# Optimization experiments

Measured on AMD Instinct MI355X. Metric: run time of the kernel, lower is better.

The kernel has to match this reference:

```python
import jax, jax.numpy as jnp
import numpy as np

EPS = 1e-5

def binary_activation(x):
    # ReActNet piecewise-polynomial STE: forward = sign(x), grad follows poly
    m1 = (x < -1).astype(x.dtype)
    m2 = (x < 0).astype(x.dtype)
    m3 = (x < 1).astype(x.dtype)
    out1 = -1.0 * m1 + (x * x + 2.0 * x) * (1.0 - m1)
    out2 = out1 * m2 + (-x * x + 2.0 * x) * (1.0 - m2)
    out3 = out2 * m3 + 1.0 * (1.0 - m3)
    return jax.lax.stop_gradient(jnp.sign(x) - out3) + out3

def binary_conv(x, w, stride, padding):
    # per-output-channel scaled sign weights with clamp STE
    scale = jnp.mean(jnp.abs(w), axis=(1, 2, 3), keepdims=True)
    clipped = jnp.clip(w, -1.0, 1.0)
    bw = jax.lax.stop_gradient(scale * jnp.sign(w) - clipped) + clipped
    return jax.lax.conv_general_dilated(
        x, bw, window_strides=(stride, stride),
        padding=[(padding, padding), (padding, padding)],
        dimension_numbers=('NCHW', 'OIHW', 'NCHW'))

def batch_norm(x, g, b):
    mu = jnp.mean(x, axis=(0, 2, 3), keepdims=True)
    var = jnp.mean((x - mu) ** 2, axis=(0, 2, 3), keepdims=True)
    xn = (x - mu) * jax.lax.rsqrt(var + EPS)
    return xn * g[None, :, None, None] + b[None, :, None, None]

def prelu(x, a):
    a = a[None, :, None, None]
    return jnp.where(x >= 0, x, a * x)

def setup_inputs() -> dict:
    key = jax.random.key(0)
    ks = jax.random.split(key, 12)
    N, C, H, W = 32, 256, 56, 56
    d = {
        'x': jax.random.normal(ks[0], (N, C, H, W), jnp.float32),
        'b11': jax.random.normal(ks[1], (1, C, 1, 1), jnp.float32) * 0.1,
        'b12': jax.random.normal(ks[2], (1, C, 1, 1), jnp.float32) * 0.1,
        'b13': jax.random.normal(ks[3], (1, C, 1, 1), jnp.float32) * 0.1,
        'b21': jax.random.normal(ks[4], (1, C, 1, 1), jnp.float32) * 0.1,
        'b22': jax.random.normal(ks[5], (1, C, 1, 1), jnp.float32) * 0.1,
        'b23': jax.random.normal(ks[6], (1, C, 1, 1), jnp.float32) * 0.1,
        'w3x3': jax.random.normal(ks[7], (C, C, 3, 3), jnp.float32) * 0.05,
        'wpw': jax.random.normal(ks[8], (C, C, 1, 1), jnp.float32) * 0.05,
        'g1': jnp.ones((C,), jnp.float32),
        'be1': jnp.zeros((C,), jnp.float32),
        'g2': jnp.ones((C,), jnp.float32),
        'be2': jnp.zeros((C,), jnp.float32),
        'p1': jnp.full((C,), 0.25, jnp.float32),
        'p2': jnp.full((C,), 0.25, jnp.float32),
    }
    return d

def reference(x, b11, b12, b13, b21, b22, b23, w3x3, wpw, g1, be1, g2, be2, p1, p2):
    # stride=1, inplanes == planes branch
    out1 = binary_activation(x + b11)
    out1 = binary_conv(out1, w3x3, stride=1, padding=1)
    out1 = batch_norm(out1, g1, be1)
    out1 = x + out1
    out1 = prelu(out1 + b12, p1) + b13
    out2 = binary_activation(out1 + b21)
    out2 = binary_conv(out2, wpw, stride=1, padding=0)
    out2 = batch_norm(out2, g2, be2)
    out2 = out2 + out1
    out2 = prelu(out2 + b22, p2) + b23
    return out2
```

## Files before the change

kernel.cpp:

```cpp
#include <hip/hip_runtime.h>

typedef __attribute__((ext_vector_type(4))) float  f32x4;
typedef __attribute__((ext_vector_type(8))) short  s16x8;
typedef __attribute__((ext_vector_type(4))) short  s16x4;
typedef __attribute__((ext_vector_type(4))) int    i32x4;

#define MFMA16(a, b, c) __builtin_amdgcn_mfma_f32_16x16x32_bf16((a), (b), (c), 0, 0, 0)

__device__ __forceinline__ void gload_lds16(const void* g, void* l) {
  __builtin_amdgcn_global_load_lds((const __attribute__((address_space(1))) void*)g,
                                   (__attribute__((address_space(3))) void*)l, 16, 0, 0);
}

__device__ __forceinline__ unsigned short sgnbits(float v) {
  return v > 0.f ? (unsigned short)0x3F80u : (v < 0.f ? (unsigned short)0xBF80u : (unsigned short)0u);
}

__global__ __launch_bounds__(256) void prep_w(const float* __restrict__ w3,
                                              const float* __restrict__ wpw,
                                              unsigned short* __restrict__ w1s,
                                              unsigned short* __restrict__ w2s,
                                              float* __restrict__ scale1,
                                              float* __restrict__ scale2) {
  const int o = blockIdx.x;
  const int t = threadIdx.x;
  float s = 0.f;
  if (blockIdx.y == 0) {
    for (int u = t; u < 2304; u += 256) {
      int i = u / 9, tap = u % 9;
      float v = w3[(size_t)(o * 256 + i) * 9 + tap];
      s += fabsf(v);
      w1s[(size_t)(tap * 256 + o) * 256 + i] = sgnbits(v);
    }
  } else {
    float v = wpw[o * 256 + t];
    s = fabsf(v);
    w2s[o * 256 + t] = sgnbits(v);
  }
  for (int m = 1; m < 64; m <<= 1) s += __shfl_xor(s, m);
  __shared__ float red[4];
  if ((t & 63) == 0) red[t >> 6] = s;
  __syncthreads();
  if (t == 0) {
    float tot = red[0] + red[1] + red[2] + red[3];
    if (blockIdx.y == 0) scale1[o] = tot / 2304.f;
    else                 scale2[o] = tot / 256.f;
  }
}

__global__ __launch_bounds__(256) void sign_nhwc(const float* __restrict__ x,
                                                 const float* __restrict__ b11,
                                                 unsigned short* __restrict__ out) {
  __shared__ unsigned short l[56 * 256];
  __shared__ float cB[256];
  const int h = blockIdx.x, n = blockIdx.y, t = threadIdx.x;
  cB[t] = b11[t];
  __syncthreads();
  const int wv = t & 15, cg = t >> 4;
  if (wv < 14) {
    const int w0 = wv * 4;
    const int swz = (wv & 7) << 3;
#pragma unroll 4
    for (int it = 0; it < 16; ++it) {
      int c = it * 16 + cg;
      size_t idx = (size_t)(n * 256 + c) * 3136 + h * 56 + w0;
      f32x4 xv = *(const f32x4*)(x + idx);
      float bb = cB[c];
      int cs = c ^ swz;
      l[(w0 + 0) * 256 + cs] = sgnbits(xv[0] + bb);
      l[(w0 + 1) * 256 + cs] = sgnbits(xv[1] + bb);
      l[(w0 + 2) * 256 + cs] = sgnbits(xv[2] + bb);
      l[(w0 + 3) * 256 + cs] = sgnbits(xv[3] + bb);
    }
  }
  __syncthreads();
  unsigned short* op = out + ((size_t)(n * 56 + h) * 56) * 256;
  for (int u = t; u < 56 * 32; u += 256) {
    int w2 = u >> 5, cp = u & 31;
    *(i32x4*)(op + w2 * 256 + cp * 8) =
        *(const i32x4*)&l[w2 * 256 + ((cp * 8) ^ (((w2 >> 2) & 7) << 3))];
  }
}

__global__ __launch_bounds__(256, 2) void conv3x3(const unsigned short* __restrict__ sIn,
                                                  const unsigned short* __restrict__ wSgn,
                                                  short* __restrict__ raw,
                                                  float* __restrict__ S,
                                                  float* __restrict__ SS) {
  __shared__ unsigned short lin[10 * 64 * 32];
  __shared__ unsigned short lw[9 * 64 * 32];

  int bid = (blockIdx.x & 7) * 112 + (blockIdx.x >> 3);
  const int ot = bid & 3;
  const int g  = bid >> 2;
  const int ht = g % 7, n = g / 7;
  const int h0 = ht * 8, oc0 = ot * 64;

  const int t = threadIdx.x;
  const int lane = t & 63, wv = t >> 6;
  const int cl = lane & 15, kk = lane >> 4;
  const int kswz = (kk ^ ((cl >> 1) & 3)) << 4;

  for (int u = t; u < 10 * 64 * 4; u += 256)
    *(i32x4*)((char*)lin + (size_t)u * 16) = (i32x4){0, 0, 0, 0};

  int q0[7];
#pragma unroll
  for (int nf = 0; nf < 7; ++nf) {
    int p = wv * 112 + nf * 16 + cl;
    q0[nf] = (p / 56) * 64 + (p % 56);
  }

  f32x4 acc[4][7];
#pragma unroll
  for (int m = 0; m < 4; ++m)
#pragma unroll
    for (int nf = 0; nf < 7; ++nf) acc[m][nf] = (f32x4){0.f, 0.f, 0.f, 0.f};

  __syncthreads();

  for (int icc = 0; icc < 8; ++icc) {
    if (t < 224) {
      const int pw = t >> 2, sl = t & 3;
      const int srcslot = sl ^ (((1 + pw) >> 1) & 3);
#pragma unroll
      for (int rr = 0; rr < 10; ++rr) {
        int h = h0 - 1 + rr;
        if (h >= 0 && h < 56) {
          const char* src = (const char*)sIn +
              ((size_t)((n * 56 + h) * 56 + pw) * 512 + icc * 64 + srcslot * 16);
          char* dst = (char*)lin + ((rr * 64 + 1) * 64 + t * 16);
          gload_lds16(src, dst);
        }
      }
    }
#pragma unroll
    for (int i = 0; i < 9; ++i) {
      int u = i * 256 + t;
      int tap = u >> 8, oc_e = (u >> 2) & 63;
      int srcslot = (u & 3) ^ ((u >> 3) & 3);
      const unsigned short* src = wSgn +
          ((size_t)(tap * 256 + oc0 + oc_e) * 256 + icc * 32 + srcslot * 8);
      gload_lds16(src, (char*)lw + (size_t)u * 16);
    }
    __syncthreads();

#pragma unroll
    for (int kh = 0; kh < 3; ++kh)
#pragma unroll
      for (int kw = 0; kw < 3; ++kw) {
        const int tap = kh * 3 + kw;
        s16x8 a[4];
#pragma unroll
        for (int m = 0; m < 4; ++m)
          a[m] = *(const s16x8*)((const char*)lw + (tap * 64 + m * 16 + cl) * 64 + kswz);
#pragma unroll
        for (int nf = 0; nf < 7; ++nf) {
          int qq = q0[nf] + kw;
          int addr = (qq + kh * 64) * 64 + ((kk ^ ((qq >> 1) & 3)) << 4);
          s16x8 b = *(const s16x8*)((const char*)lin + addr);
#pragma unroll
          for (int m = 0; m < 4; ++m) acc[m][nf] = MFMA16(a[m], b, acc[m][nf]);
        }
      }
    __syncthreads();
  }

#pragma unroll
  for (int m = 0; m < 4; ++m) {
    float sm[4] = {0.f, 0.f, 0.f, 0.f}, sq[4] = {0.f, 0.f, 0.f, 0.f};
#pragma unroll
    for (int nf = 0; nf < 7; ++nf) {
      int p = wv * 112 + nf * 16 + cl;
      int h = h0 + p / 56, w = p % 56;
      size_t base = ((size_t)n * 256 + oc0 + m * 16 + kk * 4) * 3136 + h * 56 + w;
      f32x4 v = acc[m][nf];
#pragma unroll
      for (int r2 = 0; r2 < 4; ++r2) {
        raw[base + (size_t)r2 * 3136] = (short)(int)v[r2];
        sm[r2] += v[r2];
        sq[r2] += v[r2] * v[r2];
      }
    }
#pragma unroll
    for (int r2 = 0; r2 < 4; ++r2) {
      float aa = sm[r2], qq = sq[r2];
      aa += __shfl_xor(aa, 1); qq += __shfl_xor(qq, 1);
      aa += __shfl_xor(aa, 2); qq += __shfl_xor(qq, 2);
      aa += __shfl_xor(aa, 4); qq += __shfl_xor(qq, 4);
      aa += __shfl_xor(aa, 8); qq += __shfl_xor(qq, 8);
      if (cl == 0) {
        int oc = oc0 + m * 16 + kk * 4 + r2;
        atomicAdd(&S[oc], aa);
        atomicAdd(&SS[oc], qq);
      }
    }
  }
}

__global__ __launch_bounds__(256, 2) void conv1x1(const unsigned short* __restrict__ sIn,
                                                  const unsigned short* __restrict__ wSgn,
                                                  short* __restrict__ raw,
                                                  float* __restrict__ S,
                                                  float* __restrict__ SS) {
  __shared__ unsigned short lin[2 * 112 * 32];
  __shared__ unsigned short lw[2 * 256 * 32];

  const int b = blockIdx.x;
  const int n = b / 28;
  const int hw0 = (b % 28) * 112;
  const size_t px0 = (size_t)n * 3136 + hw0;
  const int t = threadIdx.x, lane = t & 63, wv = t >> 6;
  const int cl = lane & 15, kk = lane >> 4;
  const int kswz = (kk ^ ((cl >> 1) & 3)) << 4;

#define STAGE_1x1(icc, bufi)                                                        \
  {                                                                                 \
    for (int u = t; u < 448; u += 256) {                                            \
      int srcslot = (u & 3) ^ ((u >> 3) & 3);                                       \
      const char* src = (const char*)sIn +                                          \
          ((px0 + (u >> 2)) * 512 + (icc) * 64 + srcslot * 16);                     \
      gload_lds16(src, (char*)lin + (bufi) * 7168 + u * 16);                        \
    }                                                                               \
    _Pragma("unroll")                                                               \
    for (int i = 0; i < 4; ++i) {                                                   \
      int u = i * 256 + t;                                                          \
      int srcslot = (u & 3) ^ ((u >> 3) & 3);                                       \
      const unsigned short* src = wSgn +                                            \
          ((size_t)(u >> 2) * 256 + (icc) * 32 + srcslot * 8);                      \
      gload_lds16(src, (char*)lw + (bufi) * 16384 + u * 16);                        \
    }                                                                               \
  }

  f32x4 acc[4][7];
#pragma unroll
  for (int m = 0; m < 4; ++m)
#pragma unroll
    for (int nf = 0; nf < 7; ++nf) acc[m][nf] = (f32x4){0.f, 0.f, 0.f, 0.f};

  STAGE_1x1(0, 0);
  __syncthreads();
  for (int icc = 0; icc < 8; ++icc) {
    const int cur = icc & 1;
    if (icc < 7) STAGE_1x1(icc + 1, cur ^ 1);
    s16x8 bfr[7];
#pragma unroll
    for (int nf = 0; nf < 7; ++nf)
      bfr[nf] = *(const s16x8*)((const char*)lin + cur * 7168 + (nf * 16 + cl) * 64 + kswz);
#pragma unroll
    for (int m = 0; m < 4; ++m) {
      s16x8 a = *(const s16x8*)((const char*)lw + cur * 16384 +
                                (wv * 64 + m * 16 + cl) * 64 + kswz);
#pragma unroll
      for (int nf = 0; nf < 7; ++nf) acc[m][nf] = MFMA16(a, bfr[nf], acc[m][nf]);
    }
    __syncthreads();
  }

#pragma unroll
  for (int m = 0; m < 4; ++m) {
    float sm[4] = {0.f, 0.f, 0.f, 0.f}, sq[4] = {0.f, 0.f, 0.f, 0.f};
    size_t base0 = ((size_t)n * 256 + wv * 64 + m * 16 + kk * 4) * 3136 + hw0;
#pragma unroll
    for (int nf = 0; nf < 7; ++nf) {
      f32x4 v = acc[m][nf];
#pragma unroll
      for (int r2 = 0; r2 < 4; ++r2) {
        raw[base0 + (size_t)r2 * 3136 + nf * 16 + cl] = (short)(int)v[r2];
        sm[r2] += v[r2];
        sq[r2] += v[r2] * v[r2];
      }
    }
#pragma unroll
    for (int r2 = 0; r2 < 4; ++r2) {
      float aa = sm[r2], qq = sq[r2];
      aa += __shfl_xor(aa, 1); qq += __shfl_xor(qq, 1);
      aa += __shfl_xor(aa, 2); qq += __shfl_xor(qq, 2);
      aa += __shfl_xor(aa, 4); qq += __shfl_xor(qq, 4);
      aa += __shfl_xor(aa, 8); qq += __shfl_xor(qq, 8);
      if (cl == 0) {
        int oc = wv * 64 + m * 16 + kk * 4 + r2;
        atomicAdd(&S[oc], aa);
        atomicAdd(&SS[oc], qq);
      }
    }
  }
}

__global__ void bn_coef(const float* __restrict__ S, const float* __restrict__ SS,
                        const float* __restrict__ scale, const float* __restrict__ g,
                        const float* __restrict__ be, const float* __restrict__ bext,
                        float* __restrict__ A, float* __restrict__ B) {
  int o = threadIdx.x;
  const float invN = 1.f / 100352.f;
  float mu_r  = S[o] * invN;
  float var_r = SS[o] * invN - mu_r * mu_r;
  float sc    = scale[o];
  float rstd  = rsqrtf(sc * sc * var_r + 1e-5f);
  A[o] = g[o] * rstd * sc;
  B[o] = be[o] - g[o] * rstd * sc * mu_r + bext[o];
}

__global__ __launch_bounds__(256) void mid_fuse(const short* __restrict__ raw,
                                                const float* __restrict__ x,
                                                const float* __restrict__ A1,
                                                const float* __restrict__ B1,
                                                const float* __restrict__ p1,
                                                const float* __restrict__ b13,
                                                const float* __restrict__ b21,
                                                float* __restrict__ t1,
                                                unsigned short* __restrict__ s2) {
  __shared__ unsigned short l[56 * 256];
  __shared__ float cA[256], cB[256], cP[256], cD[256], cE[256];
  const int h = blockIdx.x, n = blockIdx.y, t = threadIdx.x;
  cA[t] = A1[t]; cB[t] = B1[t]; cP[t] = p1[t]; cD[t] = b13[t]; cE[t] = b21[t];
  __syncthreads();
  const int wv = t & 15, cg = t >> 4;
  if (wv < 14) {
    const int w0 = wv * 4;
    const int swz = (wv & 7) << 3;
#pragma unroll 4
    for (int it = 0; it < 16; ++it) {
      int c = it * 16 + cg;
      size_t idx = (size_t)(n * 256 + c) * 3136 + h * 56 + w0;
      f32x4 xv = *(const f32x4*)(x + idx);
      s16x4 rv = *(const s16x4*)(raw + idx);
      float a = cA[c], b = cB[c], p = cP[c], d = cD[c], e = cE[c];
      f32x4 o;
      int cs = c ^ swz;
#pragma unroll
      for (int j = 0; j < 4; ++j) {
        float u = xv[j] + a * (float)rv[j] + b;
        u = (u >= 0.f ? u : p * u) + d;
        o[j] = u;
        l[(w0 + j) * 256 + cs] = sgnbits(u + e);
      }
      *(f32x4*)(t1 + idx) = o;
    }
  }
  __syncthreads();
  unsigned short* op = s2 + ((size_t)(n * 56 + h) * 56) * 256;
  for (int u = t; u < 56 * 32; u += 256) {
    int w2 = u >> 5, cp = u & 31;
    *(i32x4*)(op + w2 * 256 + cp * 8) =
        *(const i32x4*)&l[w2 * 256 + ((cp * 8) ^ (((w2 >> 2) & 7) << 3))];
  }
}

__global__ __launch_bounds__(256) void final_fuse(const short* __restrict__ raw,
                                                  const float* __restrict__ A2,
                                                  const float* __restrict__ B2,
                                                  const float* __restrict__ p2,
                                                  const float* __restrict__ b23,
                                                  float* out) {
  const int c = blockIdx.x & 255;
  const size_t base = (size_t)blockIdx.x * 3136;
  const float a = A2[c], b = B2[c], p = p2[c], d = b23[c];
  for (int i = threadIdx.x; i < 784; i += 256) {
    s16x4 r  = *(const s16x4*)(raw + base + (size_t)i * 4);
    f32x4 tt = *(const f32x4*)(out + base + (size_t)i * 4);
    f32x4 o;
#pragma unroll
    for (int j = 0; j < 4; ++j) {
      float v = a * (float)r[j] + b + tt[j];
      o[j] = (v >= 0.f ? v : p * v) + d;
    }
    *(f32x4*)(out + base + (size_t)i * 4) = o;
  }
}

extern "C" void kernel_launch(void* const* d_in, const int* in_sizes, int n_in,
                              void* d_out, int out_size, void* d_ws, size_t ws_size,
                              hipStream_t stream) {
  const float* x   = (const float*)d_in[0];
  const float* b11 = (const float*)d_in[1];
  const float* b12 = (const float*)d_in[2];
  const float* b13 = (const float*)d_in[3];
  const float* b21 = (const float*)d_in[4];
  const float* b22 = (const float*)d_in[5];
  const float* b23 = (const float*)d_in[6];
  const float* w3  = (const float*)d_in[7];
  const float* wpw = (const float*)d_in[8];
  const float* g1  = (const float*)d_in[9];
  const float* be1 = (const float*)d_in[10];
  const float* g2  = (const float*)d_in[11];
  const float* be2 = (const float*)d_in[12];
  const float* p1  = (const float*)d_in[13];
  const float* p2  = (const float*)d_in[14];

  char* ws = (char*)d_ws;
  short*          raw    = (short*)(ws);
  unsigned short* sgn    = (unsigned short*)(ws + 51380224);
  unsigned short* w1s    = (unsigned short*)(ws + 102760448);
  unsigned short* w2s    = (unsigned short*)(ws + 103940096);
  float*          scale1 = (float*)(ws + 104071168);
  float*          scale2 = (float*)(ws + 104072192);
  float*          S1     = (float*)(ws + 104073216);
  float*          SS1    = (float*)(ws + 104074240);
  float*          S2     = (float*)(ws + 104075264);
  float*          SS2    = (float*)(ws + 104076288);
  float*          A1     = (float*)(ws + 104077312);
  float*          B1     = (float*)(ws + 104078336);
  float*          A2     = (float*)(ws + 104079360);
  float*          B2     = (float*)(ws + 104080384);
  float*          t1     = (float*)d_out;

  hipMemsetAsync(ws + 104073216, 0, 4096, stream);

  prep_w<<<dim3(256, 2), 256, 0, stream>>>(w3, wpw, w1s, w2s, scale1, scale2);
  sign_nhwc<<<dim3(56, 32), 256, 0, stream>>>(x, b11, sgn);
  conv3x3<<<dim3(896), 256, 0, stream>>>(sgn, w1s, raw, S1, SS1);
  bn_coef<<<1, 256, 0, stream>>>(S1, SS1, scale1, g1, be1, b12, A1, B1);
  mid_fuse<<<dim3(56, 32), 256, 0, stream>>>(raw, x, A1, B1, p1, b13, b21, t1, sgn);
  conv1x1<<<dim3(896), 256, 0, stream>>>(sgn, w2s, raw, S2, SS2);
  bn_coef<<<1, 256, 0, stream>>>(S2, SS2, scale2, g2, be2, b22, A2, B2);
  final_fuse<<<dim3(8192), 256, 0, stream>>>(raw, A2, B2, p2, b23, (float*)d_out);
}
```

Measured before the change: 434.4 us.

## Switch binary convolutions from bf16 MFMA to int8 MFMA with int8 sign tensors

```diff
diff --git a/kernel.cpp b/kernel.cpp
--- a/kernel.cpp
+++ b/kernel.cpp
@@ -1,25 +1,24 @@
 #include <hip/hip_runtime.h>
 
 typedef __attribute__((ext_vector_type(4))) float  f32x4;
-typedef __attribute__((ext_vector_type(8))) short  s16x8;
 typedef __attribute__((ext_vector_type(4))) short  s16x4;
 typedef __attribute__((ext_vector_type(4))) int    i32x4;
 
-#define MFMA16(a, b, c) __builtin_amdgcn_mfma_f32_16x16x32_bf16((a), (b), (c), 0, 0, 0)
+#define MFMAI8(a, b, c) __builtin_amdgcn_mfma_i32_16x16x64_i8((a), (b), (c), 0, 0, 0)
 
 __device__ __forceinline__ void gload_lds16(const void* g, void* l) {
   __builtin_amdgcn_global_load_lds((const __attribute__((address_space(1))) void*)g,
                                    (__attribute__((address_space(3))) void*)l, 16, 0, 0);
 }
 
-__device__ __forceinline__ unsigned short sgnbits(float v) {
-  return v > 0.f ? (unsigned short)0x3F80u : (v < 0.f ? (unsigned short)0xBF80u : (unsigned short)0u);
+__device__ __forceinline__ char sgn8(float v) {
+  return v > 0.f ? (char)1 : (v < 0.f ? (char)-1 : (char)0);
 }
 
 __global__ __launch_bounds__(256) void prep_w(const float* __restrict__ w3,
                                               const float* __restrict__ wpw,
-                                              unsigned short* __restrict__ w1s,
-                                              unsigned short* __restrict__ w2s,
+                                              char* __restrict__ w1s,
+                                              char* __restrict__ w2s,
                                               float* __restrict__ scale1,
                                               float* __restrict__ scale2) {
   const int o = blockIdx.x;
@@ -30,12 +29,12 @@
       int i = u / 9, tap = u % 9;
       float v = w3[(size_t)(o * 256 + i) * 9 + tap];
       s += fabsf(v);
-      w1s[(size_t)(tap * 256 + o) * 256 + i] = sgnbits(v);
+      w1s[(size_t)(tap * 256 + o) * 256 + i] = sgn8(v);
     }
   } else {
     float v = wpw[o * 256 + t];
     s = fabsf(v);
-    w2s[o * 256 + t] = sgnbits(v);
+    w2s[o * 256 + t] = sgn8(v);
   }
   for (int m = 1; m < 64; m <<= 1) s += __shfl_xor(s, m);
   __shared__ float red[4];
@@ -50,8 +49,8 @@
 
 __global__ __launch_bounds__(256) void sign_nhwc(const float* __restrict__ x,
                                                  const float* __restrict__ b11,
-                                                 unsigned short* __restrict__ out) {
-  __shared__ unsigned short l[56 * 256];
+                                                 char* __restrict__ out) {
+  __shared__ unsigned short l[56 * 128];
   __shared__ float cB[256];
   const int h = blockIdx.x, n = blockIdx.y, t = threadIdx.x;
   cB[t] = b11[t];
@@ -61,34 +60,38 @@
     const int w0 = wv * 4;
     const int swz = (wv & 7) << 3;
 #pragma unroll 4
-    for (int it = 0; it < 16; ++it) {
-      int c = it * 16 + cg;
-      size_t idx = (size_t)(n * 256 + c) * 3136 + h * 56 + w0;
-      f32x4 xv = *(const f32x4*)(x + idx);
-      float bb = cB[c];
-      int cs = c ^ swz;
-      l[(w0 + 0) * 256 + cs] = sgnbits(xv[0] + bb);
-      l[(w0 + 1) * 256 + cs] = sgnbits(xv[1] + bb);
-      l[(w0 + 2) * 256 + cs] = sgnbits(xv[2] + bb);
-      l[(w0 + 3) * 256 + cs] = sgnbits(xv[3] + bb);
-    }
-  }
-  __syncthreads();
-  unsigned short* op = out + ((size_t)(n * 56 + h) * 56) * 256;
-  for (int u = t; u < 56 * 32; u += 256) {
-    int w2 = u >> 5, cp = u & 31;
-    *(i32x4*)(op + w2 * 256 + cp * 8) =
-        *(const i32x4*)&l[w2 * 256 + ((cp * 8) ^ (((w2 >> 2) & 7) << 3))];
-  }
-}
-
-__global__ __launch_bounds__(256, 2) void conv3x3(const unsigned short* __restrict__ sIn,
-                                                  const unsigned short* __restrict__ wSgn,
+    for (int it = 0; it < 8; ++it) {
+      int cp = it * 16 + cg;
+      int c0 = cp * 2;
+      size_t i0 = (size_t)(n * 256 + c0) * 3136 + h * 56 + w0;
+      f32x4 x0 = *(const f32x4*)(x + i0);
+      f32x4 x1 = *(const f32x4*)(x + i0 + 3136);
+      float bb0 = cB[c0], bb1 = cB[c0 + 1];
+      int cs = cp ^ swz;
+#pragma unroll
+      for (int j = 0; j < 4; ++j) {
+        unsigned short pk = (unsigned char)sgn8(x0[j] + bb0) |
+                            ((unsigned short)(unsigned char)sgn8(x1[j] + bb1) << 8);
+        l[(w0 + j) * 128 + cs] = pk;
+      }
+    }
+  }
+  __syncthreads();
+  char* op = out + ((size_t)(n * 56 + h) * 56) * 256;
+  for (int u = t; u < 56 * 16; u += 256) {
+    int w2 = u >> 4, cp = u & 15;
+    *(i32x4*)(op + w2 * 256 + cp * 16) =
+        *(const i32x4*)&l[w2 * 128 + ((cp * 8) ^ (((w2 >> 2) & 7) << 3))];
+  }
+}
+
+__global__ __launch_bounds__(256, 2) void conv3x3(const char* __restrict__ sIn,
+                                                  const char* __restrict__ wSgn,
                                                   short* __restrict__ raw,
                                                   float* __restrict__ S,
                                                   float* __restrict__ SS) {
-  __shared__ unsigned short lin[10 * 64 * 32];
-  __shared__ unsigned short lw[9 * 64 * 32];
+  __shared__ char lin[10 * 64 * 64];
+  __shared__ char lw[9 * 64 * 64];
 
   int bid = (blockIdx.x & 7) * 112 + (blockIdx.x >> 3);
   const int ot = bid & 3;
@@ -102,7 +105,7 @@
   const int kswz = (kk ^ ((cl >> 1) & 3)) << 4;
 
   for (int u = t; u < 10 * 64 * 4; u += 256)
-    *(i32x4*)((char*)lin + (size_t)u * 16) = (i32x4){0, 0, 0, 0};
+    *(i32x4*)(lin + (size_t)u * 16) = (i32x4){0, 0, 0, 0};
 
   int q0[7];
 #pragma unroll
@@ -111,15 +114,15 @@
     q0[nf] = (p / 56) * 64 + (p % 56);
   }
 
-  f32x4 acc[4][7];
+  i32x4 acc[4][7];
 #pragma unroll
   for (int m = 0; m < 4; ++m)
 #pragma unroll
-    for (int nf = 0; nf < 7; ++nf) acc[m][nf] = (f32x4){0.f, 0.f, 0.f, 0.f};
-
-  __syncthreads();
-
-  for (int icc = 0; icc < 8; ++icc) {
+    for (int nf = 0; nf < 7; ++nf) acc[m][nf] = (i32x4){0, 0, 0, 0};
+
+  __syncthreads();
+
+  for (int icc = 0; icc < 4; ++icc) {
     if (t < 224) {
       const int pw = t >> 2, sl = t & 3;
       const int srcslot = sl ^ (((1 + pw) >> 1) & 3);
@@ -127,10 +130,9 @@
       for (int rr = 0; rr < 10; ++rr) {
         int h = h0 - 1 + rr;
         if (h >= 0 && h < 56) {
-          const char* src = (const char*)sIn +
-              ((size_t)((n * 56 + h) * 56 + pw) * 512 + icc * 64 + srcslot * 16);
-          char* dst = (char*)lin + ((rr * 64 + 1) * 64 + t * 16);
-          gload_lds16(src, dst);
+          const char* src = sIn +
+              ((size_t)((n * 56 + h) * 56 + pw) * 256 + icc * 64 + srcslot * 16);
+          gload_lds16(src, lin + ((rr * 64 + 1) * 64 + t * 16));
         }
       }
     }
@@ -139,9 +141,9 @@
       int u = i * 256 + t;
       int tap = u >> 8, oc_e = (u >> 2) & 63;
       int srcslot = (u & 3) ^ ((u >> 3) & 3);
-      const unsigned short* src = wSgn +
-          ((size_t)(tap * 256 + oc0 + oc_e) * 256 + icc * 32 + srcslot * 8);
-      gload_lds16(src, (char*)lw + (size_t)u * 16);
+      const char* src = wSgn +
+          ((size_t)(tap * 256 + oc0 + oc_e) * 256 + icc * 64 + srcslot * 16);
+      gload_lds16(src, lw + (size_t)u * 16);
     }
     __syncthreads();
 
@@ -150,17 +152,17 @@
 #pragma unroll
       for (int kw = 0; kw < 3; ++kw) {
         const int tap = kh * 3 + kw;
-        s16x8 a[4];
+        i32x4 a[4];
 #pragma unroll
         for (int m = 0; m < 4; ++m)
-          a[m] = *(const s16x8*)((const char*)lw + (tap * 64 + m * 16 + cl) * 64 + kswz);
+          a[m] = *(const i32x4*)(lw + (tap * 64 + m * 16 + cl) * 64 + kswz);
 #pragma unroll
         for (int nf = 0; nf < 7; ++nf) {
           int qq = q0[nf] + kw;
           int addr = (qq + kh * 64) * 64 + ((kk ^ ((qq >> 1) & 3)) << 4);
-          s16x8 b = *(const s16x8*)((const char*)lin + addr);
-#pragma unroll
-          for (int m = 0; m < 4; ++m) acc[m][nf] = MFMA16(a[m], b, acc[m][nf]);
+          i32x4 b = *(const i32x4*)(lin + addr);
+#pragma unroll
+          for (int m = 0; m < 4; ++m) acc[m][nf] = MFMAI8(a[m], b, acc[m][nf]);
         }
       }
     __syncthreads();
@@ -174,12 +176,13 @@
       int p = wv * 112 + nf * 16 + cl;
       int h = h0 + p / 56, w = p % 56;
       size_t base = ((size_t)n * 256 + oc0 + m * 16 + kk * 4) * 3136 + h * 56 + w;
-      f32x4 v = acc[m][nf];
+      i32x4 v = acc[m][nf];
 #pragma unroll
       for (int r2 = 0; r2 < 4; ++r2) {
-        raw[base + (size_t)r2 * 3136] = (short)(int)v[r2];
-        sm[r2] += v[r2];
-        sq[r2] += v[r2] * v[r2];
+        raw[base + (size_t)r2 * 3136] = (short)v[r2];
+        float fv = (float)v[r2];
+        sm[r2] += fv;
+        sq[r2] += fv * fv;
       }
     }
 #pragma unroll
@@ -198,13 +201,13 @@
   }
 }
 
-__global__ __launch_bounds__(256, 2) void conv1x1(const unsigned short* __restrict__ sIn,
-                                                  const unsigned short* __restrict__ wSgn,
+__global__ __launch_bounds__(256, 2) void conv1x1(const char* __restrict__ sIn,
+                                                  const char* __restrict__ wSgn,
                                                   short* __restrict__ raw,
                                                   float* __restrict__ S,
                                                   float* __restrict__ SS) {
-  __shared__ unsigned short lin[2 * 112 * 32];
-  __shared__ unsigned short lw[2 * 256 * 32];
+  __shared__ char lin[2 * 112 * 64];
+  __shared__ char lw[2 * 256 * 64];
 
   const int b = blockIdx.x;
   const int n = b / 28;
@@ -218,41 +221,38 @@
   {                                                                                 \
     for (int u = t; u < 448; u += 256) {                                            \
       int srcslot = (u & 3) ^ ((u >> 3) & 3);                                       \
-      const char* src = (const char*)sIn +                                          \
-          ((px0 + (u >> 2)) * 512 + (icc) * 64 + srcslot * 16);                     \
-      gload_lds16(src, (char*)lin + (bufi) * 7168 + u * 16);                        \
+      const char* src = sIn + ((px0 + (u >> 2)) * 256 + (icc) * 64 + srcslot * 16); \
+      gload_lds16(src, lin + (bufi) * 7168 + u * 16);                               \
     }                                                                               \
     _Pragma("unroll")                                                               \
     for (int i = 0; i < 4; ++i) {                                                   \
       int u = i * 256 + t;                                                          \
       int srcslot = (u & 3) ^ ((u >> 3) & 3);                                       \
-      const unsigned short* src = wSgn +                                            \
-          ((size_t)(u >> 2) * 256 + (icc) * 32 + srcslot * 8);                      \
-      gload_lds16(src, (char*)lw + (bufi) * 16384 + u * 16);                        \
+      const char* src = wSgn + ((size_t)(u >> 2) * 256 + (icc) * 64 + srcslot * 16);\
+      gload_lds16(src, lw + (bufi) * 16384 + u * 16);                               \
     }                                                                               \
   }
 
-  f32x4 acc[4][7];
+  i32x4 acc[4][7];
 #pragma unroll
   for (int m = 0; m < 4; ++m)
 #pragma unroll
-    for (int nf = 0; nf < 7; ++nf) acc[m][nf] = (f32x4){0.f, 0.f, 0.f, 0.f};
+    for (int nf = 0; nf < 7; ++nf) acc[m][nf] = (i32x4){0, 0, 0, 0};
 
   STAGE_1x1(0, 0);
   __syncthreads();
-  for (int icc = 0; icc < 8; ++icc) {
+  for (int icc = 0; icc < 4; ++icc) {
     const int cur = icc & 1;
-    if (icc < 7) STAGE_1x1(icc + 1, cur ^ 1);
-    s16x8 bfr[7];
+    if (icc < 3) STAGE_1x1(icc + 1, cur ^ 1);
+    i32x4 bfr[7];
 #pragma unroll
     for (int nf = 0; nf < 7; ++nf)
-      bfr[nf] = *(const s16x8*)((const char*)lin + cur * 7168 + (nf * 16 + cl) * 64 + kswz);
+      bfr[nf] = *(const i32x4*)(lin + cur * 7168 + (nf * 16 + cl) * 64 + kswz);
 #pragma unroll
     for (int m = 0; m < 4; ++m) {
-      s16x8 a = *(const s16x8*)((const char*)lw + cur * 16384 +
-                                (wv * 64 + m * 16 + cl) * 64 + kswz);
-#pragma unroll
-      for (int nf = 0; nf < 7; ++nf) acc[m][nf] = MFMA16(a, bfr[nf], acc[m][nf]);
+      i32x4 a = *(const i32x4*)(lw + cur * 16384 + (wv * 64 + m * 16 + cl) * 64 + kswz);
+#pragma unroll
+      for (int nf = 0; nf < 7; ++nf) acc[m][nf] = MFMAI8(a, bfr[nf], acc[m][nf]);
     }
     __syncthreads();
   }
@@ -263,12 +263,13 @@
     size_t base0 = ((size_t)n * 256 + wv * 64 + m * 16 + kk * 4) * 3136 + hw0;
 #pragma unroll
     for (int nf = 0; nf < 7; ++nf) {
-      f32x4 v = acc[m][nf];
+      i32x4 v = acc[m][nf];
 #pragma unroll
       for (int r2 = 0; r2 < 4; ++r2) {
-        raw[base0 + (size_t)r2 * 3136 + nf * 16 + cl] = (short)(int)v[r2];
-        sm[r2] += v[r2];
-        sq[r2] += v[r2] * v[r2];
+        raw[base0 + (size_t)r2 * 3136 + nf * 16 + cl] = (short)v[r2];
+        float fv = (float)v[r2];
+        sm[r2] += fv;
+        sq[r2] += fv * fv;
       }
     }
 #pragma unroll
@@ -309,8 +310,8 @@
                                                 const float* __restrict__ b13,
                                                 const float* __restrict__ b21,
                                                 float* __restrict__ t1,
-                                                unsigned short* __restrict__ s2) {
-  __shared__ unsigned short l[56 * 256];
+                                                char* __restrict__ s2) {
+  __shared__ unsigned short l[56 * 128];
   __shared__ float cA[256], cB[256], cP[256], cD[256], cE[256];
   const int h = blockIdx.x, n = blockIdx.y, t = threadIdx.x;
   cA[t] = A1[t]; cB[t] = B1[t]; cP[t] = p1[t]; cD[t] = b13[t]; cE[t] = b21[t];
@@ -319,31 +320,41 @@
   if (wv < 14) {
     const int w0 = wv * 4;
     const int swz = (wv & 7) << 3;
-#pragma unroll 4
-    for (int it = 0; it < 16; ++it) {
-      int c = it * 16 + cg;
-      size_t idx = (size_t)(n * 256 + c) * 3136 + h * 56 + w0;
-      f32x4 xv = *(const f32x4*)(x + idx);
-      s16x4 rv = *(const s16x4*)(raw + idx);
-      float a = cA[c], b = cB[c], p = cP[c], d = cD[c], e = cE[c];
-      f32x4 o;
-      int cs = c ^ swz;
+#pragma unroll 2
+    for (int it = 0; it < 8; ++it) {
+      int cp = it * 16 + cg;
+      int c0 = cp * 2;
+      size_t i0 = (size_t)(n * 256 + c0) * 3136 + h * 56 + w0;
+      f32x4 x0 = *(const f32x4*)(x + i0);
+      f32x4 x1 = *(const f32x4*)(x + i0 + 3136);
+      s16x4 r0 = *(const s16x4*)(raw + i0);
+      s16x4 r1 = *(const s16x4*)(raw + i0 + 3136);
+      float a0 = cA[c0], b0 = cB[c0], p0 = cP[c0], d0 = cD[c0], e0 = cE[c0];
+      float a1 = cA[c0+1], b1 = cB[c0+1], p1v = cP[c0+1], d1 = cD[c0+1], e1 = cE[c0+1];
+      f32x4 o0, o1;
+      int cs = cp ^ swz;
 #pragma unroll
       for (int j = 0; j < 4; ++j) {
-        float u = xv[j] + a * (float)rv[j] + b;
-        u = (u >= 0.f ? u : p * u) + d;
-        o[j] = u;
-        l[(w0 + j) * 256 + cs] = sgnbits(u + e);
-      }
-      *(f32x4*)(t1 + idx) = o;
-    }
-  }
-  __syncthreads();
-  unsigned short* op = s2 + ((size_t)(n * 56 + h) * 56) * 256;
-  for (int u = t; u < 56 * 32; u += 256) {
-    int w2 = u >> 5, cp = u & 31;
-    *(i32x4*)(op + w2 * 256 + cp * 8) =
-        *(const i32x4*)&l[w2 * 256 + ((cp * 8) ^ (((w2 >> 2) & 7) << 3))];
+        float u0 = x0[j] + a0 * (float)r0[j] + b0;
+        u0 = (u0 >= 0.f ? u0 : p0 * u0) + d0;
+        o0[j] = u0;
+        float u1 = x1[j] + a1 * (float)r1[j] + b1;
+        u1 = (u1 >= 0.f ? u1 : p1v * u1) + d1;
+        o1[j] = u1;
+        unsigned short pk = (unsigned char)sgn8(u0 + e0) |
+                            ((unsigned short)(unsigned char)sgn8(u1 + e1) << 8);
+        l[(w0 + j) * 128 + cs] = pk;
+      }
+      *(f32x4*)(t1 + i0) = o0;
+      *(f32x4*)(t1 + i0 + 3136) = o1;
+    }
+  }
+  __syncthreads();
+  char* op = s2 + ((size_t)(n * 56 + h) * 56) * 256;
+  for (int u = t; u < 56 * 16; u += 256) {
+    int w2 = u >> 4, cp = u & 15;
+    *(i32x4*)(op + w2 * 256 + cp * 16) =
+        *(const i32x4*)&l[w2 * 128 + ((cp * 8) ^ (((w2 >> 2) & 7) << 3))];
   }
 }
 
@@ -389,23 +400,23 @@
   const float* p2  = (const float*)d_in[14];
 
   char* ws = (char*)d_ws;
-  short*          raw    = (short*)(ws);
-  unsigned short* sgn    = (unsigned short*)(ws + 51380224);
-  unsigned short* w1s    = (unsigned short*)(ws + 102760448);
-  unsigned short* w2s    = (unsigned short*)(ws + 103940096);
-  float*          scale1 = (float*)(ws + 104071168);
-  float*          scale2 = (float*)(ws + 104072192);
-  float*          S1     = (float*)(ws + 104073216);
-  float*          SS1    = (float*)(ws + 104074240);
-  float*          S2     = (float*)(ws + 104075264);
-  float*          SS2    = (float*)(ws + 104076288);
-  float*          A1     = (float*)(ws + 104077312);
-  float*          B1     = (float*)(ws + 104078336);
-  float*          A2     = (float*)(ws + 104079360);
-  float*          B2     = (float*)(ws + 104080384);
-  float*          t1     = (float*)d_out;
-
-  hipMemsetAsync(ws + 104073216, 0, 4096, stream);
+  short* raw    = (short*)(ws);
+  char*  sgn    = (char*)(ws + 51380224);
+  char*  w1s    = (char*)(ws + 77070336);
+  char*  w2s    = (char*)(ws + 77660160);
+  float* scale1 = (float*)(ws + 77725696);
+  float* scale2 = (float*)(ws + 77726720);
+  float* S1     = (float*)(ws + 77727744);
+  float* SS1    = (float*)(ws + 77728768);
+  float* S2     = (float*)(ws + 77729792);
+  float* SS2    = (float*)(ws + 77730816);
+  float* A1     = (float*)(ws + 77731840);
+  float* B1     = (float*)(ws + 77732864);
+  float* A2     = (float*)(ws + 77733888);
+  float* B2     = (float*)(ws + 77734912);
+  float* t1     = (float*)d_out;
+
+  hipMemsetAsync(ws + 77727744, 0, 4096, stream);
 
   prep_w<<<dim3(256, 2), 256, 0, stream>>>(w3, wpw, w1s, w2s, scale1, scale2);
   sign_nhwc<<<dim3(56, 32), 256, 0, stream>>>(x, b11, sgn);
```

New measurement: 385.1 us. 1.13x faster.
